# Optimization experiments

Measured on AMD Instinct MI355X. Metric: run time of the kernel, lower is better.

Reference implementation:

```python
import jax, jax.numpy as jnp
import numpy as np

N = 100000
E = 6400000
IN_CH = 128
HID = 5
H1 = 2
OUT = 10
H2 = 1
EPS_BN = 1e-5


def glorot(key, shape):
    fan = shape[0] + shape[-1]
    s = jnp.sqrt(6.0 / fan)
    return jax.random.uniform(key, shape, jnp.float32, -s, s)


def setup_inputs() -> dict:
    key = jax.random.key(0)
    ks = jax.random.split(key, 12)
    x = jax.random.normal(ks[0], (N, IN_CH), jnp.float32)
    edge_index = jax.random.randint(ks[1], (2, E), 0, N, jnp.int64)
    return {
        "x": x,
        "W1": glorot(ks[2], (IN_CH, H1 * HID)),
        "a_src1": glorot(ks[3], (H1, HID)),
        "a_dst1": glorot(ks[4], (H1, HID)),
        "b1": jnp.zeros((H1 * HID,), jnp.float32),
        "gamma1": jnp.ones((H1 * HID,), jnp.float32),
        "beta1": jnp.zeros((H1 * HID,), jnp.float32),
        "W2": glorot(ks[5], (H1 * HID, H2 * OUT)),
        "a_src2": glorot(ks[6], (H2, OUT)),
        "a_dst2": glorot(ks[7], (H2, OUT)),
        "b2": jnp.zeros((OUT,), jnp.float32),
        "edge_index": edge_index,
    }


def gat_conv(x, src, dst, W, a_src, a_dst, bias, heads, out_ch, concat):
    n = x.shape[0]
    h = (x @ W).reshape(n, heads, out_ch)          # [N,H,C]
    alpha_s = (h * a_src).sum(-1)                  # [N,H]
    alpha_d = (h * a_dst).sum(-1)                  # [N,H]
    e = jax.nn.leaky_relu(alpha_s[src] + alpha_d[dst], 0.2)  # [E,H]
    emax = jax.ops.segment_max(e, dst, num_segments=n)
    emax = jnp.where(jnp.isfinite(emax), emax, 0.0)
    ex = jnp.exp(e - jax.lax.stop_gradient(emax)[dst])
    denom = jax.ops.segment_sum(ex, dst, num_segments=n)
    alpha = ex / (denom[dst] + 1e-16)              # edge softmax by target
    msg = h[src] * alpha[..., None]                # [E,H,C]
    out = jax.ops.segment_sum(msg, dst, num_segments=n)
    out = out.reshape(n, heads * out_ch) if concat else out.mean(axis=1)
    return out + bias


def batch_norm(x, gamma, beta):
    mu = x.mean(0)
    var = ((x - mu) ** 2).mean(0)
    return (x - mu) * jax.lax.rsqrt(var + EPS_BN) * gamma + beta


def reference(x, W1, a_src1, a_dst1, b1, gamma1, beta1, W2, a_src2, a_dst2, b2, edge_index):
    n = x.shape[0]
    loop = jnp.arange(n, dtype=edge_index.dtype)   # add_self_loops=True
    src = jnp.concatenate([edge_index[0], loop])
    dst = jnp.concatenate([edge_index[1], loop])
    h = gat_conv(x, src, dst, W1, a_src1, a_dst1, b1, H1, HID, True)
    h = batch_norm(h, gamma1, beta1)
    h = jax.nn.elu(h)
    out = gat_conv(h, src, dst, W2, a_src2, a_dst2, b2, H2, OUT, False)
    return out
```

## Files before the change

### kernel.cpp

```cpp
#include <hip/hip_runtime.h>
#include <hip/hip_fp16.h>
#include <math.h>

#define NN 100000
#define NE 6400000
#define INCH 128
#define BSH 7
#define BW (1 << BSH)
#define NBKT ((NN + BW - 1) / BW)
#define NBP 784
#define BCAP 9216
#define BIN_CH 8192
#define BNP 800

__device__ inline float pkh(float a, float b) {
  __half2 h = __floats2half2_rn(a, b);
  return __uint_as_float(*reinterpret_cast<unsigned int*>(&h));
}
__device__ inline float2 uph(float f) {
  unsigned int b = __float_as_uint(f);
  __half2 h = *reinterpret_cast<__half2*>(&b);
  return __half22float2(h);
}

__global__ __launch_bounds__(512) void k_count(const int* __restrict__ ei,
                                               int* __restrict__ cntmat) {
  __shared__ int cnt4[4][NBKT];
  int t = threadIdx.x;
  int w = (t >> 6) & 3;
  for (int i = t; i < 4 * NBKT; i += 512) (&cnt4[0][0])[i] = 0;
  __syncthreads();
  int c0 = blockIdx.x * BIN_CH;
  int c1 = c0 + BIN_CH < NE ? c0 + BIN_CH : NE;
  int n4 = (c1 - c0) >> 2;
  const int4* d4 = (const int4*)(ei + NE + c0);
  for (int k = t; k < n4; k += 512) {
    int4 v = d4[k];
    atomicAdd(&cnt4[w][v.x >> BSH], 1);
    atomicAdd(&cnt4[w][v.y >> BSH], 1);
    atomicAdd(&cnt4[w][v.z >> BSH], 1);
    atomicAdd(&cnt4[w][v.w >> BSH], 1);
  }
  __syncthreads();
  for (int b = t; b < NBKT; b += 512)
    cntmat[(size_t)b * NBP + blockIdx.x] =
        cnt4[0][b] + cnt4[1][b] + cnt4[2][b] + cnt4[3][b];
}

__global__ __launch_bounds__(64) void k_scanb(const int* __restrict__ cntmat,
                                              int* __restrict__ basemat,
                                              int* __restrict__ bcnt) {
  int j = blockIdx.x;
  int lane = threadIdx.x;
  int carry = 0;
  for (int i0 = 0; i0 < NBKT; i0 += 64) {
    int i = i0 + lane;
    int v0 = (i < NBKT) ? cntmat[(size_t)j * NBP + i] : 0;
    int v = v0;
#pragma unroll
    for (int off = 1; off < 64; off <<= 1) {
      int u = __shfl_up(v, off, 64);
      if (lane >= off) v += u;
    }
    if (i < NBKT) basemat[(size_t)i * NBP + j] = carry + v - v0;
    carry += __shfl(v, 63, 64);
  }
  if (lane == 0) bcnt[j] = carry;
}

__global__ __launch_bounds__(1024) void k_scatter2(
    const int* __restrict__ ei, const int* __restrict__ cntmat,
    const int* __restrict__ basemat, unsigned int* __restrict__ pairs) {
  __shared__ int offs[NBKT];
  __shared__ int cur[NBKT];
  __shared__ int gbase[NBKT];
  __shared__ int scanp[1024];
  __shared__ unsigned int stage[BIN_CH];
  __shared__ unsigned short sbkt[BIN_CH];
  int t = threadIdx.x;
  int chunk = blockIdx.x;
  int myb0 = t * 4;
  int tots[4];
  int asum = 0;
#pragma unroll
  for (int j = 0; j < 4; j++) {
    int b = myb0 + j;
    int tt = (b < NBKT) ? cntmat[(size_t)b * NBP + chunk] : 0;
    tots[j] = tt;
    asum += tt;
  }
  for (int b = t; b < NBKT; b += 1024)
    gbase[b] = basemat[(size_t)chunk * NBP + b];
  scanp[t] = asum;
  __syncthreads();
  for (int off = 1; off < 1024; off <<= 1) {
    int v = (t >= off) ? scanp[t - off] : 0;
    __syncthreads();
    scanp[t] += v;
    __syncthreads();
  }
  int run = (t == 0) ? 0 : scanp[t - 1];
#pragma unroll
  for (int j = 0; j < 4; j++) {
    int b = myb0 + j;
    if (b < NBKT) {
      offs[b] = run;
      cur[b] = run;
      run += tots[j];
    }
  }
  __syncthreads();
  int c0 = chunk * BIN_CH;
  int c1 = c0 + BIN_CH < NE ? c0 + BIN_CH : NE;
  for (int i = c0 + t; i < c1; i += 1024) {
    int s = ei[i], d = ei[NE + i];
    int bkt = d >> BSH;
    int pos = atomicAdd(&cur[bkt], 1);
    stage[pos] = ((unsigned int)s << BSH) | (unsigned int)(d & (BW - 1));
    sbkt[pos] = (unsigned short)bkt;
  }
  __syncthreads();
  int total = c1 - c0;
  for (int i = t; i < total; i += 1024) {
    unsigned int e = stage[i];
    int b = sbkt[i];
    int gp = gbase[b] + (i - offs[b]);
    if (gp < BCAP) pairs[(size_t)b * BCAP + gp] = e;
  }
}

__global__ __launch_bounds__(1024) void k_sortb(
    const int* __restrict__ bcnt, unsigned int* __restrict__ pairs,
    unsigned int* __restrict__ oc) {
  __shared__ int cnt16[16][BW];
  __shared__ int wb16[16][BW];
  __shared__ int tot[BW];
  __shared__ int scanbuf[BW];
  __shared__ unsigned int sorted[BCAP];
  int t = threadIdx.x;
  int w = t >> 6;
  int b = blockIdx.x;
  int base_n = b << BSH;
  for (int i = t; i < 16 * BW; i += 1024) (&cnt16[0][0])[i] = 0;
  __syncthreads();
  int cntb = bcnt[b];
  cntb = cntb > BCAP ? BCAP : cntb;
  unsigned int* pp = pairs + (size_t)b * BCAP;
  for (int k = t; k < cntb; k += 1024)
    atomicAdd(&cnt16[w][pp[k] & (BW - 1)], 1);
  __syncthreads();
  if (t < BW) {
    int tt = 0;
#pragma unroll
    for (int j = 0; j < 16; j++) tt += cnt16[j][t];
    tot[t] = tt;
    scanbuf[t] = tt;
  }
  __syncthreads();
  for (int step = 1; step < BW; step <<= 1) {
    int v = 0;
    if (t < BW && t >= step) v = scanbuf[t - step];
    __syncthreads();
    if (t < BW) scanbuf[t] += v;
    __syncthreads();
  }
  if (t < BW) {
    int run = scanbuf[t] - tot[t];
    int n = base_n + t;
    if (n < NN) oc[n] = ((unsigned int)run << 16) | (unsigned int)tot[t];
#pragma unroll
    for (int j = 0; j < 16; j++) { wb16[j][t] = run; run += cnt16[j][t]; cnt16[j][t] = 0; }
  }
  __syncthreads();
  for (int k = t; k < cntb; k += 1024) {
    unsigned int e = pp[k];
    int dl = e & (BW - 1);
    int pos = wb16[w][dl] + atomicAdd(&cnt16[w][dl], 1);
    sorted[pos] = e >> BSH;
  }
  __syncthreads();
  for (int k = t; k < cntb; k += 1024) pp[k] = sorted[k];
}

__global__ __launch_bounds__(256) void k_l1_node(
    const float* __restrict__ x, const float* __restrict__ W1,
    const float* __restrict__ a_src1, const float* __restrict__ a_dst1,
    float* __restrict__ h1, float2* __restrict__ ad1) {
  __shared__ float Wt[10 * INCH];
  __shared__ float asw[10], adw[10];
  for (int i = threadIdx.x; i < 10 * INCH; i += blockDim.x) {
    int c = i / 10, k = i - c * 10;
    Wt[k * INCH + c] = W1[i];
  }
  if (threadIdx.x < 10) {
    asw[threadIdx.x] = a_src1[threadIdx.x];
    adw[threadIdx.x] = a_dst1[threadIdx.x];
  }
  __syncthreads();
  int n = blockIdx.x * blockDim.x + threadIdx.x;
  if (n >= NN) return;
  const float4* xr = (const float4*)(x + (size_t)n * INCH);
  const float4* Wt4 = (const float4*)Wt;
  float acc[10];
#pragma unroll
  for (int k = 0; k < 10; k++) acc[k] = 0.f;
#pragma unroll 8
  for (int c4 = 0; c4 < INCH / 4; c4++) {
    float4 xv = xr[c4];
#pragma unroll
    for (int k = 0; k < 10; k++) {
      float4 wv = Wt4[k * (INCH / 4) + c4];
      acc[k] += xv.x * wv.x + xv.y * wv.y + xv.z * wv.z + xv.w * wv.w;
    }
  }
  float s0 = 0.f, s1 = 0.f, d0 = 0.f, d1 = 0.f;
#pragma unroll
  for (int j = 0; j < 5; j++) {
    s0 += acc[j] * asw[j];
    s1 += acc[5 + j] * asw[5 + j];
    d0 += acc[j] * adw[j];
    d1 += acc[5 + j] * adw[5 + j];
  }
  float4* hrow = (float4*)(h1 + (size_t)n * 8);
  hrow[0] = make_float4(pkh(acc[0], acc[1]), pkh(acc[2], acc[3]),
                        pkh(acc[4], acc[5]), pkh(acc[6], acc[7]));
  hrow[1] = make_float4(pkh(acc[8], acc[9]), 0.f, s0, s1);
  ad1[n] = make_float2(d0, d1);
}

__global__ __launch_bounds__(512, 8) void k_l1_aggs(
    const int* __restrict__ bcnt,
    const unsigned int* __restrict__ sorted_g, const unsigned int* __restrict__ oc,
    const float* __restrict__ h1, const float2* __restrict__ ad1,
    const float* __restrict__ b1, float* __restrict__ g1,
    float* __restrict__ bn_part) {
  __shared__ __align__(16) unsigned int sorted[BCAP];
  __shared__ float biasS[10];
  __shared__ float bn_lds[8 * 20];
  int t = threadIdx.x;
  int w = t >> 6;
  int b = blockIdx.x;
  int base_n = b << BSH;
  if (t < 10) biasS[t] = b1[t];
  {
    int cb = bcnt[b];
    cb = cb > BCAP ? BCAP : cb;
    int n4 = (cb + 3) >> 2;
    const uint4* pp4 = (const uint4*)(sorted_g + (size_t)b * BCAP);
    uint4* s4 = (uint4*)sorted;
    for (int k = t; k < n4; k += 512) s4[k] = pp4[k];
  }
  __syncthreads();
  int node = t >> 2;
  int part = t & 3;
  int n = base_n + node;
  bool valid = n < NN;
  unsigned int ocv = valid ? oc[n] : 0u;
  int s0i = (int)(ocv >> 16);
  int c = (int)(ocv & 0xffffu);
  float2 adn = valid ? ad1[n] : make_float2(0.f, 0.f);
  float acc[10];
#pragma unroll
  for (int j = 0; j < 10; j++) acc[j] = 0.f;
  float den0 = 0.f, den1 = 0.f;
#pragma unroll 2
  for (int k = part; k < c; k += 4) {
    int s = (int)sorted[s0i + k];
    const float4* hs = (const float4*)(h1 + (size_t)s * 8);
    float4 ra = hs[0], rb = hs[1];
    float e0 = rb.z + adn.x; e0 = e0 > 0.f ? e0 : 0.2f * e0;
    float e1 = rb.w + adn.y; e1 = e1 > 0.f ? e1 : 0.2f * e1;
    float x0 = __expf(e0), x1 = __expf(e1);
    float2 h01 = uph(ra.x), h23 = uph(ra.y), h45 = uph(ra.z), h67 = uph(ra.w),
           h89 = uph(rb.x);
    acc[0] += x0 * h01.x;  acc[1] += x0 * h01.y;  acc[2] += x0 * h23.x;
    acc[3] += x0 * h23.y;  acc[4] += x0 * h45.x;
    acc[5] += x1 * h45.y;  acc[6] += x1 * h67.x;  acc[7] += x1 * h67.y;
    acc[8] += x1 * h89.x;  acc[9] += x1 * h89.y;
    den0 += x0; den1 += x1;
  }
#pragma unroll
  for (int j = 0; j < 10; j++) {
    acc[j] += __shfl_xor(acc[j], 1, 64);
    acc[j] += __shfl_xor(acc[j], 2, 64);
  }
  den0 += __shfl_xor(den0, 1, 64); den0 += __shfl_xor(den0, 2, 64);
  den1 += __shfl_xor(den1, 1, 64); den1 += __shfl_xor(den1, 2, 64);
  float v[10];
#pragma unroll
  for (int j = 0; j < 10; j++) v[j] = 0.f;
  if (part == 0 && valid) {
    const float4* hs = (const float4*)(h1 + (size_t)n * 8);
    float4 ra = hs[0], rb = hs[1];
    float e0 = rb.z + adn.x; e0 = e0 > 0.f ? e0 : 0.2f * e0;
    float e1 = rb.w + adn.y; e1 = e1 > 0.f ? e1 : 0.2f * e1;
    float x0 = __expf(e0), x1 = __expf(e1);
    float2 h01 = uph(ra.x), h23 = uph(ra.y), h45 = uph(ra.z), h67 = uph(ra.w),
           h89 = uph(rb.x);
    acc[0] += x0 * h01.x;  acc[1] += x0 * h01.y;  acc[2] += x0 * h23.x;
    acc[3] += x0 * h23.y;  acc[4] += x0 * h45.x;
    acc[5] += x1 * h45.y;  acc[6] += x1 * h67.x;  acc[7] += x1 * h67.y;
    acc[8] += x1 * h89.x;  acc[9] += x1 * h89.y;
    den0 += x0; den1 += x1;
    float i0 = 1.f / (den0 + 1e-16f), i1 = 1.f / (den1 + 1e-16f);
#pragma unroll
    for (int j = 0; j < 5; j++) v[j] = acc[j] * i0 + biasS[j];
#pragma unroll
    for (int j = 5; j < 10; j++) v[j] = acc[j] * i1 + biasS[j];
    float4* gr = (float4*)(g1 + (size_t)n * 12);
    gr[0] = make_float4(v[0], v[1], v[2], v[3]);
    gr[1] = make_float4(v[4], v[5], v[6], v[7]);
    gr[2] = make_float4(v[8], v[9], 0.f, 0.f);
  }
  float s[20];
#pragma unroll
  for (int j = 0; j < 10; j++) { s[j] = v[j]; s[10 + j] = v[j] * v[j]; }
#pragma unroll
  for (int j = 0; j < 20; j++) {
    s[j] += __shfl_down(s[j], 4, 64);
    s[j] += __shfl_down(s[j], 8, 64);
    s[j] += __shfl_down(s[j], 16, 64);
    s[j] += __shfl_down(s[j], 32, 64);
  }
  if ((t & 63) == 0) {
#pragma unroll
    for (int j = 0; j < 20; j++) bn_lds[w * 20 + j] = s[j];
  }
  __syncthreads();
  if (t == 0) {
#pragma unroll
    for (int j = 0; j < 20; j++) {
      float acc20 = 0.f;
#pragma unroll
      for (int ww = 0; ww < 8; ww++) acc20 += bn_lds[ww * 20 + j];
      bn_part[j * BNP + b] = acc20;
    }
  }
}

__global__ __launch_bounds__(64) void k_bnred(const float* __restrict__ bn_part,
                                              float* __restrict__ bns) {
  int j = blockIdx.x;
  int lane = threadIdx.x;
  float s = 0.f;
  for (int b = lane; b < NBKT; b += 64) s += bn_part[j * BNP + b];
#pragma unroll
  for (int off = 32; off > 0; off >>= 1) s += __shfl_down(s, off, 64);
  if (lane == 0) bns[j] = s;
}

__global__ __launch_bounds__(256) void k_l2_node(
    const float* __restrict__ g1, const float* __restrict__ bns,
    const float* __restrict__ gamma1, const float* __restrict__ beta1,
    const float* __restrict__ W2, const float* __restrict__ a_src2,
    const float* __restrict__ a_dst2, float* __restrict__ h2,
    float* __restrict__ ad2) {
  __shared__ float scale[10], shift[10], W2s[100], a2s[10], a2d[10];
  if (threadIdx.x < 10) {
    int j = threadIdx.x;
    float mu = bns[j] * (1.f / NN);
    float var = bns[10 + j] * (1.f / NN) - mu * mu;
    float rs = rsqrtf(var + 1e-5f);
    scale[j] = rs * gamma1[j];
    shift[j] = beta1[j] - mu * rs * gamma1[j];
    a2s[j] = a_src2[j];
    a2d[j] = a_dst2[j];
  }
  for (int i = threadIdx.x; i < 100; i += blockDim.x) W2s[i] = W2[i];
  __syncthreads();
  int n = blockIdx.x * blockDim.x + threadIdx.x;
  if (n >= NN) return;
  const float4* gr = (const float4*)(g1 + (size_t)n * 12);
  float4 g0 = gr[0], g1v = gr[1], g2 = gr[2];
  float hv[10] = {g0.x, g0.y, g0.z, g0.w, g1v.x, g1v.y, g1v.z, g1v.w, g2.x, g2.y};
#pragma unroll
  for (int j = 0; j < 10; j++) {
    float t = hv[j] * scale[j] + shift[j];
    hv[j] = t > 0.f ? t : (__expf(t) - 1.f);
  }
  float o[10];
#pragma unroll
  for (int k = 0; k < 10; k++) o[k] = 0.f;
#pragma unroll
  for (int c = 0; c < 10; c++) {
#pragma unroll
    for (int k = 0; k < 10; k++) o[k] += hv[c] * W2s[c * 10 + k];
  }
  float ss = 0.f, sd = 0.f;
#pragma unroll
  for (int k = 0; k < 10; k++) { ss += o[k] * a2s[k]; sd += o[k] * a2d[k]; }
  float4* hr = (float4*)(h2 + (size_t)n * 8);
  hr[0] = make_float4(pkh(o[0], o[1]), pkh(o[2], o[3]), pkh(o[4], o[5]),
                      pkh(o[6], o[7]));
  hr[1] = make_float4(pkh(o[8], o[9]), 0.f, ss, 0.f);
  ad2[n] = sd;
}

__global__ __launch_bounds__(512, 8) void k_l2_aggs(
    const int* __restrict__ bcnt,
    const unsigned int* __restrict__ sorted_g, const unsigned int* __restrict__ oc,
    const float* __restrict__ h2, const float* __restrict__ ad2,
    const float* __restrict__ b2, float* __restrict__ out) {
  __shared__ __align__(16) unsigned int sorted[BCAP];
  __shared__ float biasS[10];
  int t = threadIdx.x;
  int b = blockIdx.x;
  int base_n = b << BSH;
  if (t < 10) biasS[t] = b2[t];
  {
    int cb = bcnt[b];
    cb = cb > BCAP ? BCAP : cb;
    int n4 = (cb + 3) >> 2;
    const uint4* pp4 = (const uint4*)(sorted_g + (size_t)b * BCAP);
    uint4* s4 = (uint4*)sorted;
    for (int k = t; k < n4; k += 512) s4[k] = pp4[k];
  }
  __syncthreads();
  int node = t >> 2;
  int part = t & 3;
  int n = base_n + node;
  bool valid = n < NN;
  unsigned int ocv = valid ? oc[n] : 0u;
  int s0i = (int)(ocv >> 16);
  int c = (int)(ocv & 0xffffu);
  float adn = valid ? ad2[n] : 0.f;
  float acc[10];
#pragma unroll
  for (int j = 0; j < 10; j++) acc[j] = 0.f;
  float den = 0.f;
#pragma unroll 2
  for (int k = part; k < c; k += 4) {
    int s = (int)sorted[s0i + k];
    const float4* hs = (const float4*)(h2 + (size_t)s * 8);
    float4 ra = hs[0], rb = hs[1];
    float ee = rb.z + adn; ee = ee > 0.f ? ee : 0.2f * ee;
    float xv = __expf(ee);
    float2 h01 = uph(ra.x), h23 = uph(ra.y), h45 = uph(ra.z), h67 = uph(ra.w),
           h89 = uph(rb.x);
    acc[0] += xv * h01.x;  acc[1] += xv * h01.y;  acc[2] += xv * h23.x;
    acc[3] += xv * h23.y;  acc[4] += xv * h45.x;  acc[5] += xv * h45.y;
    acc[6] += xv * h67.x;  acc[7] += xv * h67.y;  acc[8] += xv * h89.x;
    acc[9] += xv * h89.y;
    den += xv;
  }
#pragma unroll
  for (int j = 0; j < 10; j++) {
    acc[j] += __shfl_xor(acc[j], 1, 64);
    acc[j] += __shfl_xor(acc[j], 2, 64);
  }
  den += __shfl_xor(den, 1, 64); den += __shfl_xor(den, 2, 64);
  if (part == 0 && valid) {
    const float4* hs = (const float4*)(h2 + (size_t)n * 8);
    float4 ra = hs[0], rb = hs[1];
    float ee = rb.z + adn; ee = ee > 0.f ? ee : 0.2f * ee;
    float xv = __expf(ee);
    float2 h01 = uph(ra.x), h23 = uph(ra.y), h45 = uph(ra.z), h67 = uph(ra.w),
           h89 = uph(rb.x);
    acc[0] += xv * h01.x;  acc[1] += xv * h01.y;  acc[2] += xv * h23.x;
    acc[3] += xv * h23.y;  acc[4] += xv * h45.x;  acc[5] += xv * h45.y;
    acc[6] += xv * h67.x;  acc[7] += xv * h67.y;  acc[8] += xv * h89.x;
    acc[9] += xv * h89.y;
    den += xv;
    float inv = 1.f / (den + 1e-16f);
    float2* orow = (float2*)(out + (size_t)n * 10);
    orow[0] = make_float2(acc[0] * inv + biasS[0], acc[1] * inv + biasS[1]);
    orow[1] = make_float2(acc[2] * inv + biasS[2], acc[3] * inv + biasS[3]);
    orow[2] = make_float2(acc[4] * inv + biasS[4], acc[5] * inv + biasS[5]);
    orow[3] = make_float2(acc[6] * inv + biasS[6], acc[7] * inv + biasS[7]);
    orow[4] = make_float2(acc[8] * inv + biasS[8], acc[9] * inv + biasS[9]);
  }
}

extern "C" void kernel_launch(void* const* d_in, const int* in_sizes, int n_in,
                              void* d_out, int out_size, void* d_ws, size_t ws_size,
                              hipStream_t stream) {
  const float* x      = (const float*)d_in[0];
  const float* W1     = (const float*)d_in[1];
  const float* a_src1 = (const float*)d_in[2];
  const float* a_dst1 = (const float*)d_in[3];
  const float* b1     = (const float*)d_in[4];
  const float* gamma1 = (const float*)d_in[5];
  const float* beta1  = (const float*)d_in[6];
  const float* W2     = (const float*)d_in[7];
  const float* a_src2 = (const float*)d_in[8];
  const float* a_dst2 = (const float*)d_in[9];
  const float* b2     = (const float*)d_in[10];
  const int*   ei     = (const int*)d_in[11];
  float* out = (float*)d_out;

  int* bcnt = (int*)d_ws;
  unsigned int* pairs = (unsigned int*)d_ws + 1024;
  float* h1 = (float*)(pairs + (size_t)NBKT * BCAP);
  float* ad1 = h1 + (size_t)NN * 8;
  float* g1 = ad1 + (size_t)NN * 2;
  float* h2 = g1 + (size_t)NN * 12;
  float* ad2 = h2 + (size_t)NN * 8;
  float* bn_part = ad2 + NN;
  float* bns = bn_part + 20 * BNP;
  int* cntmat = (int*)(bns + 20 + 12);
  int* basemat = cntmat + (size_t)NBKT * NBP;
  unsigned int* oc = (unsigned int*)(basemat + (size_t)NBKT * NBP);

  const int B = 256;
  const int gN = (NN + B - 1) / B;
  const int gBin = (NE + BIN_CH - 1) / BIN_CH;

  k_count<<<gBin, 512, 0, stream>>>(ei, cntmat);
  k_scanb<<<NBKT, 64, 0, stream>>>(cntmat, basemat, bcnt);
  k_scatter2<<<gBin, 1024, 0, stream>>>(ei, cntmat, basemat, pairs);
  k_sortb<<<NBKT, 1024, 0, stream>>>(bcnt, pairs, oc);
  k_l1_node<<<gN, B, 0, stream>>>(x, W1, a_src1, a_dst1, h1, (float2*)ad1);
  k_l1_aggs<<<NBKT, 512, 0, stream>>>(bcnt, pairs, oc, h1, (const float2*)ad1,
                                      b1, g1, bn_part);
  k_bnred<<<20, 64, 0, stream>>>(bn_part, bns);
  k_l2_node<<<gN, B, 0, stream>>>(g1, bns, gamma1, beta1, W2, a_src2, a_dst2,
                                  h2, ad2);
  k_l2_aggs<<<NBKT, 512, 0, stream>>>(bcnt, pairs, oc, h2, ad2, b2, out);
}
```

Baseline: 330.2 us.

## Split each gathered neighbor row across lane pairs in both aggregation kernels

Both edge-aggregation kernels now give each edge to a pair of lanes: each lane loads one 16-byte half of the 32-byte source row, the odd lane computes the exp and shuffles it to its partner, and accumulators are split between the two lanes. Each node now gets 8 lanes (4 edge slots × 2 halves), and the block covers its 128 nodes in two passes. The aim is narrower per-lane memory requests and less register pressure in the gather loop. In exchange it adds extra shuffles, divergent work between odd and even lanes, and a second pass over nodes per block.

```diff
diff --git a/kernel.cpp b/kernel.cpp
--- a/kernel.cpp
+++ b/kernel.cpp
@@ -251,80 +251,97 @@
     for (int k = t; k < n4; k += 512) s4[k] = pp4[k];
   }
   __syncthreads();
-  int node = t >> 2;
-  int part = t & 3;
-  int n = base_n + node;
-  bool valid = n < NN;
-  unsigned int ocv = valid ? oc[n] : 0u;
-  int s0i = (int)(ocv >> 16);
-  int c = (int)(ocv & 0xffffu);
-  float2 adn = valid ? ad1[n] : make_float2(0.f, 0.f);
-  float acc[10];
-#pragma unroll
-  for (int j = 0; j < 10; j++) acc[j] = 0.f;
-  float den0 = 0.f, den1 = 0.f;
-#pragma unroll 2
-  for (int k = part; k < c; k += 4) {
-    int s = (int)sorted[s0i + k];
-    const float4* hs = (const float4*)(h1 + (size_t)s * 8);
-    float4 ra = hs[0], rb = hs[1];
-    float e0 = rb.z + adn.x; e0 = e0 > 0.f ? e0 : 0.2f * e0;
-    float e1 = rb.w + adn.y; e1 = e1 > 0.f ? e1 : 0.2f * e1;
-    float x0 = __expf(e0), x1 = __expf(e1);
-    float2 h01 = uph(ra.x), h23 = uph(ra.y), h45 = uph(ra.z), h67 = uph(ra.w),
-           h89 = uph(rb.x);
-    acc[0] += x0 * h01.x;  acc[1] += x0 * h01.y;  acc[2] += x0 * h23.x;
-    acc[3] += x0 * h23.y;  acc[4] += x0 * h45.x;
-    acc[5] += x1 * h45.y;  acc[6] += x1 * h67.x;  acc[7] += x1 * h67.y;
-    acc[8] += x1 * h89.x;  acc[9] += x1 * h89.y;
-    den0 += x0; den1 += x1;
-  }
-#pragma unroll
-  for (int j = 0; j < 10; j++) {
-    acc[j] += __shfl_xor(acc[j], 1, 64);
-    acc[j] += __shfl_xor(acc[j], 2, 64);
-  }
-  den0 += __shfl_xor(den0, 1, 64); den0 += __shfl_xor(den0, 2, 64);
-  den1 += __shfl_xor(den1, 1, 64); den1 += __shfl_xor(den1, 2, 64);
-  float v[10];
-#pragma unroll
-  for (int j = 0; j < 10; j++) v[j] = 0.f;
-  if (part == 0 && valid) {
-    const float4* hs = (const float4*)(h1 + (size_t)n * 8);
-    float4 ra = hs[0], rb = hs[1];
-    float e0 = rb.z + adn.x; e0 = e0 > 0.f ? e0 : 0.2f * e0;
-    float e1 = rb.w + adn.y; e1 = e1 > 0.f ? e1 : 0.2f * e1;
-    float x0 = __expf(e0), x1 = __expf(e1);
-    float2 h01 = uph(ra.x), h23 = uph(ra.y), h45 = uph(ra.z), h67 = uph(ra.w),
-           h89 = uph(rb.x);
-    acc[0] += x0 * h01.x;  acc[1] += x0 * h01.y;  acc[2] += x0 * h23.x;
-    acc[3] += x0 * h23.y;  acc[4] += x0 * h45.x;
-    acc[5] += x1 * h45.y;  acc[6] += x1 * h67.x;  acc[7] += x1 * h67.y;
-    acc[8] += x1 * h89.x;  acc[9] += x1 * h89.y;
-    den0 += x0; den1 += x1;
-    float i0 = 1.f / (den0 + 1e-16f), i1 = 1.f / (den1 + 1e-16f);
-#pragma unroll
-    for (int j = 0; j < 5; j++) v[j] = acc[j] * i0 + biasS[j];
-#pragma unroll
-    for (int j = 5; j < 10; j++) v[j] = acc[j] * i1 + biasS[j];
-    float4* gr = (float4*)(g1 + (size_t)n * 12);
-    gr[0] = make_float4(v[0], v[1], v[2], v[3]);
-    gr[1] = make_float4(v[4], v[5], v[6], v[7]);
-    gr[2] = make_float4(v[8], v[9], 0.f, 0.f);
-  }
-  float s[20];
-#pragma unroll
-  for (int j = 0; j < 10; j++) { s[j] = v[j]; s[10 + j] = v[j] * v[j]; }
+  int lane = t & 63;
+  int odd = t & 1;
+  int pairIdx = (t >> 1) & 3;
+  int gb1 = (lane & 56) | 1;
+  float bnv[20];
+#pragma unroll
+  for (int j = 0; j < 20; j++) bnv[j] = 0.f;
+  for (int half = 0; half < 2; half++) {
+    int node = half * 64 + (t >> 3);
+    int n = base_n + node;
+    bool valid = n < NN;
+    unsigned int ocv = valid ? oc[n] : 0u;
+    int s0i = (int)(ocv >> 16);
+    int c = (int)(ocv & 0xffffu);
+    float2 adn = valid ? ad1[n] : make_float2(0.f, 0.f);
+    float r0 = 0.f, r1 = 0.f, r2 = 0.f, r3 = 0.f,
+          r4 = 0.f, r5 = 0.f, r6 = 0.f, r7 = 0.f;
+    for (int k = pairIdx; k < c; k += 4) {
+      int s = (int)sorted[s0i + k];
+      const float4* hs = (const float4*)(h1 + (size_t)s * 8);
+      float4 rv = hs[odd];
+      float e0 = rv.z + adn.x; e0 = e0 > 0.f ? e0 : 0.2f * e0;
+      float e1 = rv.w + adn.y; e1 = e1 > 0.f ? e1 : 0.2f * e1;
+      float x0 = __expf(e0), x1 = __expf(e1);
+      x0 = __shfl(x0, lane | 1, 64);
+      x1 = __shfl(x1, lane | 1, 64);
+      float2 ha = uph(rv.x);
+      if (odd) {
+        r0 += x1 * ha.x;
+        r1 += x1 * ha.y;
+        r2 += x0;
+        r3 += x1;
+      } else {
+        float2 h23 = uph(rv.y), h45 = uph(rv.z), h67 = uph(rv.w);
+        r0 += x0 * ha.x;  r1 += x0 * ha.y;  r2 += x0 * h23.x;
+        r3 += x0 * h23.y; r4 += x0 * h45.x;
+        r5 += x1 * h45.y; r6 += x1 * h67.x; r7 += x1 * h67.y;
+      }
+    }
+#pragma unroll
+    for (int off = 2; off <= 4; off <<= 1) {
+      r0 += __shfl_xor(r0, off, 64); r1 += __shfl_xor(r1, off, 64);
+      r2 += __shfl_xor(r2, off, 64); r3 += __shfl_xor(r3, off, 64);
+      r4 += __shfl_xor(r4, off, 64); r5 += __shfl_xor(r5, off, 64);
+      r6 += __shfl_xor(r6, off, 64); r7 += __shfl_xor(r7, off, 64);
+    }
+    float q8 = __shfl(r0, gb1, 64);
+    float q9 = __shfl(r1, gb1, 64);
+    float qd0 = __shfl(r2, gb1, 64);
+    float qd1 = __shfl(r3, gb1, 64);
+    float v[10];
+#pragma unroll
+    for (int j = 0; j < 10; j++) v[j] = 0.f;
+    if ((t & 7) == 0 && valid) {
+      const float4* hs = (const float4*)(h1 + (size_t)n * 8);
+      float4 ra = hs[0], rb = hs[1];
+      float e0 = rb.z + adn.x; e0 = e0 > 0.f ? e0 : 0.2f * e0;
+      float e1 = rb.w + adn.y; e1 = e1 > 0.f ? e1 : 0.2f * e1;
+      float x0 = __expf(e0), x1 = __expf(e1);
+      float2 h01 = uph(ra.x), h23 = uph(ra.y), h45 = uph(ra.z),
+             h67 = uph(ra.w), h89 = uph(rb.x);
+      float a0 = r0 + x0 * h01.x, a1 = r1 + x0 * h01.y;
+      float a2 = r2 + x0 * h23.x, a3 = r3 + x0 * h23.y;
+      float a4 = r4 + x0 * h45.x, a5 = r5 + x1 * h45.y;
+      float a6 = r6 + x1 * h67.x, a7 = r7 + x1 * h67.y;
+      float a8 = q8 + x1 * h89.x, a9 = q9 + x1 * h89.y;
+      float den0 = qd0 + x0, den1 = qd1 + x1;
+      float i0 = 1.f / (den0 + 1e-16f), i1 = 1.f / (den1 + 1e-16f);
+      v[0] = a0 * i0 + biasS[0]; v[1] = a1 * i0 + biasS[1];
+      v[2] = a2 * i0 + biasS[2]; v[3] = a3 * i0 + biasS[3];
+      v[4] = a4 * i0 + biasS[4];
+      v[5] = a5 * i1 + biasS[5]; v[6] = a6 * i1 + biasS[6];
+      v[7] = a7 * i1 + biasS[7]; v[8] = a8 * i1 + biasS[8];
+      v[9] = a9 * i1 + biasS[9];
+      float4* gr = (float4*)(g1 + (size_t)n * 12);
+      gr[0] = make_float4(v[0], v[1], v[2], v[3]);
+      gr[1] = make_float4(v[4], v[5], v[6], v[7]);
+      gr[2] = make_float4(v[8], v[9], 0.f, 0.f);
+    }
+#pragma unroll
+    for (int j = 0; j < 10; j++) { bnv[j] += v[j]; bnv[10 + j] += v[j] * v[j]; }
+  }
 #pragma unroll
   for (int j = 0; j < 20; j++) {
-    s[j] += __shfl_down(s[j], 4, 64);
-    s[j] += __shfl_down(s[j], 8, 64);
-    s[j] += __shfl_down(s[j], 16, 64);
-    s[j] += __shfl_down(s[j], 32, 64);
+    bnv[j] += __shfl_down(bnv[j], 8, 64);
+    bnv[j] += __shfl_down(bnv[j], 16, 64);
+    bnv[j] += __shfl_down(bnv[j], 32, 64);
   }
   if ((t & 63) == 0) {
 #pragma unroll
-    for (int j = 0; j < 20; j++) bn_lds[w * 20 + j] = s[j];
+    for (int j = 0; j < 20; j++) bn_lds[w * 20 + j] = bnv[j];
   }
   __syncthreads();
   if (t == 0) {
@@ -416,58 +433,70 @@
     for (int k = t; k < n4; k += 512) s4[k] = pp4[k];
   }
   __syncthreads();
-  int node = t >> 2;
-  int part = t & 3;
-  int n = base_n + node;
-  bool valid = n < NN;
-  unsigned int ocv = valid ? oc[n] : 0u;
-  int s0i = (int)(ocv >> 16);
-  int c = (int)(ocv & 0xffffu);
-  float adn = valid ? ad2[n] : 0.f;
-  float acc[10];
-#pragma unroll
-  for (int j = 0; j < 10; j++) acc[j] = 0.f;
-  float den = 0.f;
-#pragma unroll 2
-  for (int k = part; k < c; k += 4) {
-    int s = (int)sorted[s0i + k];
-    const float4* hs = (const float4*)(h2 + (size_t)s * 8);
-    float4 ra = hs[0], rb = hs[1];
-    float ee = rb.z + adn; ee = ee > 0.f ? ee : 0.2f * ee;
-    float xv = __expf(ee);
-    float2 h01 = uph(ra.x), h23 = uph(ra.y), h45 = uph(ra.z), h67 = uph(ra.w),
-           h89 = uph(rb.x);
-    acc[0] += xv * h01.x;  acc[1] += xv * h01.y;  acc[2] += xv * h23.x;
-    acc[3] += xv * h23.y;  acc[4] += xv * h45.x;  acc[5] += xv * h45.y;
-    acc[6] += xv * h67.x;  acc[7] += xv * h67.y;  acc[8] += xv * h89.x;
-    acc[9] += xv * h89.y;
-    den += xv;
-  }
-#pragma unroll
-  for (int j = 0; j < 10; j++) {
-    acc[j] += __shfl_xor(acc[j], 1, 64);
-    acc[j] += __shfl_xor(acc[j], 2, 64);
-  }
-  den += __shfl_xor(den, 1, 64); den += __shfl_xor(den, 2, 64);
-  if (part == 0 && valid) {
-    const float4* hs = (const float4*)(h2 + (size_t)n * 8);
-    float4 ra = hs[0], rb = hs[1];
-    float ee = rb.z + adn; ee = ee > 0.f ? ee : 0.2f * ee;
-    float xv = __expf(ee);
-    float2 h01 = uph(ra.x), h23 = uph(ra.y), h45 = uph(ra.z), h67 = uph(ra.w),
-           h89 = uph(rb.x);
-    acc[0] += xv * h01.x;  acc[1] += xv * h01.y;  acc[2] += xv * h23.x;
-    acc[3] += xv * h23.y;  acc[4] += xv * h45.x;  acc[5] += xv * h45.y;
-    acc[6] += xv * h67.x;  acc[7] += xv * h67.y;  acc[8] += xv * h89.x;
-    acc[9] += xv * h89.y;
-    den += xv;
-    float inv = 1.f / (den + 1e-16f);
-    float2* orow = (float2*)(out + (size_t)n * 10);
-    orow[0] = make_float2(acc[0] * inv + biasS[0], acc[1] * inv + biasS[1]);
-    orow[1] = make_float2(acc[2] * inv + biasS[2], acc[3] * inv + biasS[3]);
-    orow[2] = make_float2(acc[4] * inv + biasS[4], acc[5] * inv + biasS[5]);
-    orow[3] = make_float2(acc[6] * inv + biasS[6], acc[7] * inv + biasS[7]);
-    orow[4] = make_float2(acc[8] * inv + biasS[8], acc[9] * inv + biasS[9]);
+  int lane = t & 63;
+  int odd = t & 1;
+  int pairIdx = (t >> 1) & 3;
+  int gb1 = (lane & 56) | 1;
+  for (int half = 0; half < 2; half++) {
+    int node = half * 64 + (t >> 3);
+    int n = base_n + node;
+    bool valid = n < NN;
+    unsigned int ocv = valid ? oc[n] : 0u;
+    int s0i = (int)(ocv >> 16);
+    int c = (int)(ocv & 0xffffu);
+    float adn = valid ? ad2[n] : 0.f;
+    float r0 = 0.f, r1 = 0.f, r2 = 0.f, r3 = 0.f,
+          r4 = 0.f, r5 = 0.f, r6 = 0.f, r7 = 0.f;
+    for (int k = pairIdx; k < c; k += 4) {
+      int s = (int)sorted[s0i + k];
+      const float4* hs = (const float4*)(h2 + (size_t)s * 8);
+      float4 rv = hs[odd];
+      float ee = rv.z + adn; ee = ee > 0.f ? ee : 0.2f * ee;
+      float xv = __expf(ee);
+      xv = __shfl(xv, lane | 1, 64);
+      float2 ha = uph(rv.x);
+      if (odd) {
+        r0 += xv * ha.x;
+        r1 += xv * ha.y;
+        r2 += xv;
+      } else {
+        float2 h23 = uph(rv.y), h45 = uph(rv.z), h67 = uph(rv.w);
+        r0 += xv * ha.x;  r1 += xv * ha.y;  r2 += xv * h23.x;
+        r3 += xv * h23.y; r4 += xv * h45.x; r5 += xv * h45.y;
+        r6 += xv * h67.x; r7 += xv * h67.y;
+      }
+    }
+#pragma unroll
+    for (int off = 2; off <= 4; off <<= 1) {
+      r0 += __shfl_xor(r0, off, 64); r1 += __shfl_xor(r1, off, 64);
+      r2 += __shfl_xor(r2, off, 64); r3 += __shfl_xor(r3, off, 64);
+      r4 += __shfl_xor(r4, off, 64); r5 += __shfl_xor(r5, off, 64);
+      r6 += __shfl_xor(r6, off, 64); r7 += __shfl_xor(r7, off, 64);
+    }
+    float q8 = __shfl(r0, gb1, 64);
+    float q9 = __shfl(r1, gb1, 64);
+    float qd = __shfl(r2, gb1, 64);
+    if ((t & 7) == 0 && valid) {
+      const float4* hs = (const float4*)(h2 + (size_t)n * 8);
+      float4 ra = hs[0], rb = hs[1];
+      float ee = rb.z + adn; ee = ee > 0.f ? ee : 0.2f * ee;
+      float xv = __expf(ee);
+      float2 h01 = uph(ra.x), h23 = uph(ra.y), h45 = uph(ra.z),
+             h67 = uph(ra.w), h89 = uph(rb.x);
+      float a0 = r0 + xv * h01.x, a1 = r1 + xv * h01.y;
+      float a2 = r2 + xv * h23.x, a3 = r3 + xv * h23.y;
+      float a4 = r4 + xv * h45.x, a5 = r5 + xv * h45.y;
+      float a6 = r6 + xv * h67.x, a7 = r7 + xv * h67.y;
+      float a8 = q8 + xv * h89.x, a9 = q9 + xv * h89.y;
+      float den = qd + xv;
+      float inv = 1.f / (den + 1e-16f);
+      float2* orow = (float2*)(out + (size_t)n * 10);
+      orow[0] = make_float2(a0 * inv + biasS[0], a1 * inv + biasS[1]);
+      orow[1] = make_float2(a2 * inv + biasS[2], a3 * inv + biasS[3]);
+      orow[2] = make_float2(a4 * inv + biasS[4], a5 * inv + biasS[5]);
+      orow[3] = make_float2(a6 * inv + biasS[6], a7 * inv + biasS[7]);
+      orow[4] = make_float2(a8 * inv + biasS[8], a9 * inv + biasS[9]);
+    }
   }
 }
 
```

Measured after the change: 382.8 us. +15.9%, slower.
